# Kernel optimization log

Measured on AMD Instinct MI355X. Metric: run time of the kernel, lower is better.

## Reference

```python
import jax, jax.numpy as jnp
import numpy as np

NUM_GRAPHS = 128


def _gcn_layer(x, W, b, src, dst, out_norm, in_norm, n_nodes):
    # DGL GraphConv, norm='both': x * outdeg^{-1/2}, sum-aggregate src->dst, * indeg^{-1/2}, then @W + b
    x = x * out_norm[:, None]
    agg = jax.ops.segment_sum(x[src], dst, num_segments=n_nodes)  # [N, d]
    agg = agg * in_norm[:, None]
    return agg @ W + b


def setup_inputs() -> dict:
    key = jax.random.key(0)
    ks = jax.random.split(key, 10)
    N, E, D, H, P, C = 100000, 1600000, 128, 128, 64, 10
    h = jax.random.normal(ks[0], (N, D), dtype=jnp.float32)
    perm_features = jax.random.normal(ks[1], (NUM_GRAPHS, P), dtype=jnp.float32)
    W1 = jax.random.normal(ks[2], (D, H), dtype=jnp.float32) * (1.0 / np.sqrt(D))
    b1 = jnp.zeros((H,), dtype=jnp.float32)
    W2 = jax.random.normal(ks[3], (H, H), dtype=jnp.float32) * (1.0 / np.sqrt(H))
    b2 = jnp.zeros((H,), dtype=jnp.float32)
    Wc = jax.random.normal(ks[4], (H + P, C), dtype=jnp.float32) * (1.0 / np.sqrt(H + P))
    bc = jnp.zeros((C,), dtype=jnp.float32)
    src = jax.random.randint(ks[5], (E,), 0, N, dtype=jnp.int64)
    dst = jax.random.randint(ks[6], (E,), 0, N, dtype=jnp.int64)
    graph_ids = jnp.sort(jax.random.randint(ks[7], (N,), 0, NUM_GRAPHS, dtype=jnp.int64))
    return {"h": h, "perm_features": perm_features, "W1": W1, "b1": b1,
            "W2": W2, "b2": b2, "Wc": Wc, "bc": bc,
            "src": src, "dst": dst, "graph_ids": graph_ids}


def reference(h, perm_features, W1, b1, W2, b2, Wc, bc, src, dst, graph_ids):
    N = h.shape[0]
    ones_e = jnp.ones(src.shape[0], dtype=h.dtype)
    out_deg = jnp.maximum(jax.ops.segment_sum(ones_e, src, num_segments=N), 1.0)
    in_deg = jnp.maximum(jax.ops.segment_sum(ones_e, dst, num_segments=N), 1.0)
    out_norm = jax.lax.rsqrt(out_deg)
    in_norm = jax.lax.rsqrt(in_deg)

    x = _gcn_layer(h, W1, b1, src, dst, out_norm, in_norm, N)
    x = jax.nn.relu(x)
    x = _gcn_layer(x, W2, b2, src, dst, out_norm, in_norm, N)

    # dgl.mean_nodes: per-graph mean of node features
    sums = jax.ops.segment_sum(x, graph_ids, num_segments=NUM_GRAPHS)  # [G, H]
    counts = jnp.maximum(
        jax.ops.segment_sum(jnp.ones(N, dtype=x.dtype), graph_ids, num_segments=NUM_GRAPHS), 1.0)
    hg = sums / counts[:, None]

    combined = jnp.concatenate([hg, perm_features], axis=1)  # [G, H+P]
    return combined @ Wc + bc
```

## Files before the change

kernel.cpp:

```cpp
#include <hip/hip_runtime.h>


#define NUM_G 128
#define PB_EDGES 4096
#define W_BIN 128

typedef unsigned int uint32;
typedef short bf16x8 __attribute__((ext_vector_type(8)));
typedef float f32x4 __attribute__((ext_vector_type(4)));

__device__ __forceinline__ float bflo(uint32 u) { return __uint_as_float(u << 16); }
__device__ __forceinline__ float bfhi(uint32 u) { return __uint_as_float(u & 0xffff0000u); }
__device__ __forceinline__ uint32 f2bf_bits(float f) {
    uint32 b = __float_as_uint(f);
    return (b + 0x7fffu + ((b >> 16) & 1u)) >> 16;
}
__device__ __forceinline__ uint32 pack2(float a, float b) {
    return f2bf_bits(a) | (f2bf_bits(b) << 16);
}

__global__ __launch_bounds__(256) void p1_hist(const int* __restrict__ src,
                                               const int* __restrict__ dst, int E,
                                               int NBIN, int B, int* __restrict__ bh) {
    __shared__ int hist[1024];
    int b = blockIdx.x;
    int pipe = (b >= B) ? 1 : 0;
    int bb = pipe ? b - B : b;
    const int* key = pipe ? src : dst;
    for (int i = threadIdx.x; i < NBIN; i += 256) hist[i] = 0;
    __syncthreads();
    int base = bb * PB_EDGES;
    for (int c = threadIdx.x; c < PB_EDGES / 4; c += 256) {
        int e = base + c * 4;
        if (e + 3 < E) {
            int4 k4 = *(const int4*)(key + e);
            atomicAdd(&hist[k4.x >> 7], 1);
            atomicAdd(&hist[k4.y >> 7], 1);
            atomicAdd(&hist[k4.z >> 7], 1);
            atomicAdd(&hist[k4.w >> 7], 1);
        } else {
            for (int i = e; i < E && i < e + 4; i++) atomicAdd(&hist[key[i] >> 7], 1);
        }
    }
    __syncthreads();
    int* outp = bh + (size_t)pipe * NBIN * B;
    for (int k = threadIdx.x; k < NBIN; k += 256)
        outp[(size_t)k * B + bb] = hist[k];
}

__global__ __launch_bounds__(256) void p2a_tot(const int* __restrict__ bh, int NBIN, int B,
                                               int* __restrict__ tot) {
    __shared__ int sc[256];
    int k = blockIdx.x % NBIN, pipe = blockIdx.x / NBIN;
    const int* row = bh + (size_t)pipe * NBIN * B + (size_t)k * B;
    int acc = 0;
    for (int b = threadIdx.x; b < B; b += 256) acc += row[b];
    sc[threadIdx.x] = acc;
    __syncthreads();
    for (int o = 128; o > 0; o >>= 1) {
        if (threadIdx.x < o) sc[threadIdx.x] += sc[threadIdx.x + o];
        __syncthreads();
    }
    if (threadIdx.x == 0) tot[pipe * NBIN + k] = sc[0];
}

__global__ __launch_bounds__(512) void p2c_cursor(const int* __restrict__ bh,
                                                  const int* __restrict__ tot,
                                                  int NBIN, int B, int E,
                                                  int* __restrict__ bstart,
                                                  int* __restrict__ curs) {
    __shared__ int sc[512];
    int k = blockIdx.x % NBIN, pipe = blockIdx.x / NBIN;
    int i = threadIdx.x;
    int pacc = 0;
    for (int kk = i; kk < k; kk += 512) pacc += tot[pipe * NBIN + kk];
    sc[i] = pacc;
    __syncthreads();
    for (int o = 256; o > 0; o >>= 1) {
        if (i < o) sc[i] += sc[i + o];
        __syncthreads();
    }
    int base = sc[0];
    __syncthreads();
    if (i == 0) {
        bstart[pipe * (NBIN + 1) + k] = base;
        if (k == 0) bstart[pipe * (NBIN + 1) + NBIN] = E;
    }
    const int* row = bh + (size_t)pipe * NBIN * B + (size_t)k * B;
    int v = (i < B) ? row[i] : 0;
    sc[i] = v;
    __syncthreads();
    for (int o = 1; o < 512; o <<= 1) {
        int t = (i >= o) ? sc[i - o] : 0;
        __syncthreads();
        sc[i] += t;
        __syncthreads();
    }
    if (i < B)
        curs[(size_t)pipe * B * NBIN + (size_t)i * NBIN + k] = base + sc[i] - v;
}

__global__ __launch_bounds__(256) void p3_scatter(const int* __restrict__ src,
                                                  const int* __restrict__ dst, int E,
                                                  int NBIN, int B, const int* __restrict__ curs,
                                                  int* __restrict__ ebuf, int* __restrict__ sbuf) {
    __shared__ int cur[1024];
    int b = blockIdx.x;
    int pipe = (b >= B) ? 1 : 0;
    int bb = pipe ? b - B : b;
    const int* crow = curs + (size_t)pipe * B * NBIN + (size_t)bb * NBIN;
    for (int i = threadIdx.x; i < NBIN; i += 256) cur[i] = crow[i];
    __syncthreads();
    int base = bb * PB_EDGES;
    if (!pipe) {
        for (int c = threadIdx.x; c < PB_EDGES / 4; c += 256) {
            int e = base + c * 4;
            if (e + 3 < E) {
                int4 s4 = *(const int4*)(src + e);
                int4 d4 = *(const int4*)(dst + e);
                int p;
                p = atomicAdd(&cur[d4.x >> 7], 1); ebuf[p] = s4.x | ((d4.x & 127) << 17);
                p = atomicAdd(&cur[d4.y >> 7], 1); ebuf[p] = s4.y | ((d4.y & 127) << 17);
                p = atomicAdd(&cur[d4.z >> 7], 1); ebuf[p] = s4.z | ((d4.z & 127) << 17);
                p = atomicAdd(&cur[d4.w >> 7], 1); ebuf[p] = s4.w | ((d4.w & 127) << 17);
            } else {
                for (int i = e; i < E && i < e + 4; i++) {
                    int s = src[i], d = dst[i];
                    int p = atomicAdd(&cur[d >> 7], 1);
                    ebuf[p] = s | ((d & 127) << 17);
                }
            }
        }
    } else {
        for (int c = threadIdx.x; c < PB_EDGES / 4; c += 256) {
            int e = base + c * 4;
            if (e + 3 < E) {
                int4 s4 = *(const int4*)(src + e);
                int p;
                p = atomicAdd(&cur[s4.x >> 7], 1); sbuf[p] = s4.x;
                p = atomicAdd(&cur[s4.y >> 7], 1); sbuf[p] = s4.y;
                p = atomicAdd(&cur[s4.z >> 7], 1); sbuf[p] = s4.z;
                p = atomicAdd(&cur[s4.w >> 7], 1); sbuf[p] = s4.w;
            } else {
                for (int i = e; i < E && i < e + 4; i++) {
                    int s = src[i];
                    int p = atomicAdd(&cur[s >> 7], 1);
                    sbuf[p] = s;
                }
            }
        }
    }
}

__global__ __launch_bounds__(256) void p4_comb(const int* __restrict__ ebuf,
                                               const int* __restrict__ sbuf,
                                               const int* __restrict__ bstart,
                                               int NBIN, int N, int E,
                                               int* __restrict__ indeg, int* __restrict__ coff,
                                               int* __restrict__ adj, int* __restrict__ outdeg) {
    __shared__ int hist[128];
    __shared__ int sc[128];
    __shared__ int cur[128];
    __shared__ int lsrc[4096];
    int kb = blockIdx.x;
    int tid = threadIdx.x;
    if (kb >= NBIN) {
        int k = kb - NBIN;
        const int* bstartS = bstart + (NBIN + 1);
        int s0 = bstartS[k], s1 = bstartS[k + 1];
        if (tid < 128) hist[tid] = 0;
        __syncthreads();
        for (int i = s0 + tid; i < s1; i += 256) atomicAdd(&hist[sbuf[i] & 127], 1);
        __syncthreads();
        if (tid < 128) {
            int node = k * W_BIN + tid;
            if (node < N) outdeg[node] = hist[tid];
        }
        return;
    }
    int k = kb;
    int s0 = bstart[k], s1 = bstart[k + 1];
    int M = s1 - s0;
    if (tid < 128) hist[tid] = 0;
    __syncthreads();
    for (int i = tid; i < M; i += 256) {
        int e = ebuf[s0 + i];
        atomicAdd(&hist[(e >> 17) & 127], 1);
    }
    __syncthreads();
    if (tid < 128) sc[tid] = hist[tid];
    __syncthreads();
    for (int o = 1; o < 128; o <<= 1) {
        int v = 0;
        if (tid < 128 && tid >= o) v = sc[tid - o];
        __syncthreads();
        if (tid < 128) sc[tid] += v;
        __syncthreads();
    }
    if (tid < 128) {
        int node = k * W_BIN + tid;
        if (node < N) {
            indeg[node] = hist[tid];
            coff[node] = s0 + sc[tid] - hist[tid];
        }
        cur[tid] = sc[tid] - hist[tid];
    }
    if (k == NBIN - 1 && tid == 0) coff[N] = E;
    __syncthreads();
    if (M <= 4096) {
        for (int i = tid; i < M; i += 256) {
            int e = ebuf[s0 + i];
            int p = atomicAdd(&cur[(e >> 17) & 127], 1);
            lsrc[p] = e & 0x1FFFF;
        }
        __syncthreads();
        for (int i = tid; i < M; i += 256) adj[s0 + i] = lsrc[i];
    } else {
        for (int i = tid; i < M; i += 256) {
            int e = ebuf[s0 + i];
            int p = atomicAdd(&cur[(e >> 17) & 127], 1);
            adj[s0 + p] = e & 0x1FFFF;
        }
    }
}

__global__ void misc_kernel(const int* __restrict__ gids,
                            const int* __restrict__ outdeg, const int* __restrict__ indeg,
                            const float* __restrict__ W1, const float* __restrict__ W2,
                            int N, int* __restrict__ goffs,
                            float* __restrict__ nrm_out, float* __restrict__ nrm_in,
                            unsigned short* __restrict__ Wt1, unsigned short* __restrict__ Wt2) {
    int i = blockIdx.x * blockDim.x + threadIdx.x;
    if (i <= N) {
        int prev = (i == 0) ? -1 : gids[i - 1];
        int cur = (i == N) ? NUM_G : gids[i];
        for (int g = prev + 1; g <= cur && g <= NUM_G; g++) goffs[g] = i;
    }
    if (i < N) {
        nrm_out[i] = rsqrtf(fmaxf((float)outdeg[i], 1.0f));
        nrm_in[i]  = rsqrtf(fmaxf((float)indeg[i], 1.0f));
    }
    if (i < 32768) {
        int sel = i >> 14;
        int idx = i & 16383;
        int k = idx >> 7, n = idx & 127;
        float v = (sel ? W2 : W1)[idx];
        (sel ? Wt2 : Wt1)[n * 128 + k] = (unsigned short)f2bf_bits(v);
    }
}

__global__ void scale_kernel(const float* __restrict__ h, const float* __restrict__ nrm_out,
                             uint32* __restrict__ xsb, int N) {
    int t = blockIdx.x * blockDim.x + threadIdx.x;
    int node = t >> 4, q = t & 15;
    if (node >= N) return;
    float ns = nrm_out[node];
    const float4* hv = (const float4*)(h + (size_t)node * 128 + q * 8);
    float4 a = hv[0], b = hv[1];
    a.x *= ns; a.y *= ns; a.z *= ns; a.w *= ns;
    b.x *= ns; b.y *= ns; b.z *= ns; b.w *= ns;
    uint4 o;
    o.x = pack2(a.x, a.y); o.y = pack2(a.z, a.w);
    o.z = pack2(b.x, b.y); o.w = pack2(b.z, b.w);
    ((uint4*)xsb)[(size_t)node * 16 + q] = o;
}

__device__ __forceinline__ void acc8(float* acc, uint4 u) {
    acc[0] += bflo(u.x); acc[1] += bfhi(u.x); acc[2] += bflo(u.y); acc[3] += bfhi(u.y);
    acc[4] += bflo(u.z); acc[5] += bfhi(u.z); acc[6] += bflo(u.w); acc[7] += bfhi(u.w);
}

__global__ void agg_kernel(const uint32* __restrict__ xsb, const int* __restrict__ adj,
                           const int* __restrict__ coff, uint32* __restrict__ aggb, int N) {
    int t = blockIdx.x * blockDim.x + threadIdx.x;
    int node = t >> 4;
    int q = t & 15;
    if (node >= N) return;
    int jb = coff[node], je = coff[node + 1];
    float acc[8];
#pragma unroll
    for (int i = 0; i < 8; i++) acc[i] = 0.f;
    const uint4* rows = (const uint4*)xsb;
    int j = jb;
    for (; j + 7 < je; j += 8) {
        int s0 = adj[j], s1 = adj[j + 1], s2 = adj[j + 2], s3 = adj[j + 3];
        int s4 = adj[j + 4], s5 = adj[j + 5], s6 = adj[j + 6], s7 = adj[j + 7];
        uint4 u0 = rows[(size_t)s0 * 16 + q];
        uint4 u1 = rows[(size_t)s1 * 16 + q];
        uint4 u2 = rows[(size_t)s2 * 16 + q];
        uint4 u3 = rows[(size_t)s3 * 16 + q];
        uint4 u4 = rows[(size_t)s4 * 16 + q];
        uint4 u5 = rows[(size_t)s5 * 16 + q];
        uint4 u6 = rows[(size_t)s6 * 16 + q];
        uint4 u7 = rows[(size_t)s7 * 16 + q];
        acc8(acc, u0); acc8(acc, u1); acc8(acc, u2); acc8(acc, u3);
        acc8(acc, u4); acc8(acc, u5); acc8(acc, u6); acc8(acc, u7);
    }
    for (; j + 3 < je; j += 4) {
        int s0 = adj[j], s1 = adj[j + 1], s2 = adj[j + 2], s3 = adj[j + 3];
        uint4 u0 = rows[(size_t)s0 * 16 + q];
        uint4 u1 = rows[(size_t)s1 * 16 + q];
        uint4 u2 = rows[(size_t)s2 * 16 + q];
        uint4 u3 = rows[(size_t)s3 * 16 + q];
        acc8(acc, u0); acc8(acc, u1); acc8(acc, u2); acc8(acc, u3);
    }
    for (; j < je; j++) {
        uint4 u = rows[(size_t)adj[j] * 16 + q];
        acc8(acc, u);
    }
    uint4 o;
    o.x = pack2(acc[0], acc[1]); o.y = pack2(acc[2], acc[3]);
    o.z = pack2(acc[4], acc[5]); o.w = pack2(acc[6], acc[7]);
    ((uint4*)aggb)[(size_t)node * 16 + q] = o;
}

__global__ __launch_bounds__(256) void gemm_mfma(const unsigned short* __restrict__ A,
                                                 const unsigned short* __restrict__ Wtg,
                                                 const float* __restrict__ bias,
                                                 const float* __restrict__ rowscale,
                                                 const float* __restrict__ postscale,
                                                 unsigned short* __restrict__ out,
                                                 int N, int do_relu) {
    __shared__ unsigned short Wl[128 * 136];
    for (int i = threadIdx.x; i < 2048; i += 256) {
        uint4 v = ((const uint4*)Wtg)[i];
        *(uint4*)&Wl[(i >> 4) * 136 + (i & 15) * 8] = v;
    }
    __syncthreads();

    int lane = threadIdx.x & 63;
    int wv = threadIdx.x >> 6;
    int col_l = lane & 15;
    int quad = lane >> 4;
    int r0w = blockIdx.x * 128 + wv * 32;
    if (r0w >= N) return;

    int arow0 = r0w + col_l;        if (arow0 >= N) arow0 = N - 1;
    int arow1 = r0w + 16 + col_l;   if (arow1 >= N) arow1 = N - 1;
    const unsigned short* Ar0 = A + (size_t)arow0 * 128;
    const unsigned short* Ar1 = A + (size_t)arow1 * 128;

    f32x4 acc[2][8];
#pragma unroll
    for (int rt = 0; rt < 2; rt++)
#pragma unroll
        for (int t = 0; t < 8; t++) {
            acc[rt][t][0] = 0.f; acc[rt][t][1] = 0.f;
            acc[rt][t][2] = 0.f; acc[rt][t][3] = 0.f;
        }

#pragma unroll
    for (int kk = 0; kk < 4; kk++) {
        bf16x8 a0 = *(const bf16x8*)(Ar0 + kk * 32 + quad * 8);
        bf16x8 a1 = *(const bf16x8*)(Ar1 + kk * 32 + quad * 8);
        const unsigned short* wb = &Wl[(size_t)col_l * 136 + kk * 32 + quad * 8];
#pragma unroll
        for (int t = 0; t < 8; t++) {
            bf16x8 b = *(const bf16x8*)(wb + (size_t)t * 16 * 136);
            acc[0][t] = __builtin_amdgcn_mfma_f32_16x16x32_bf16(a0, b, acc[0][t], 0, 0, 0);
            acc[1][t] = __builtin_amdgcn_mfma_f32_16x16x32_bf16(a1, b, acc[1][t], 0, 0, 0);
        }
    }

#pragma unroll
    for (int rt = 0; rt < 2; rt++) {
        int rbase = r0w + rt * 16;
        float s[4], p[4];
#pragma unroll
        for (int j = 0; j < 4; j++) {
            int rw = rbase + quad * 4 + j;
            bool ok = rw < N;
            s[j] = ok ? rowscale[ok ? rw : 0] : 0.f;
            p[j] = (postscale != nullptr && ok) ? postscale[rw] : 1.f;
        }
#pragma unroll
        for (int t = 0; t < 8; t++) {
            int c = t * 16 + col_l;
            float bia = bias[c];
#pragma unroll
            for (int j = 0; j < 4; j++) {
                int rw = rbase + quad * 4 + j;
                if (rw >= N) continue;
                float v = fmaf(s[j], acc[rt][t][j], bia);
                if (do_relu) v = fmaxf(v, 0.f);
                v *= p[j];
                out[(size_t)rw * 128 + c] = (unsigned short)f2bf_bits(v);
            }
        }
    }
}

__global__ __launch_bounds__(1024) void mean_final(const uint32* __restrict__ x2b,
                                                   const int* __restrict__ goffs,
                                                   const float* __restrict__ perm,
                                                   const float* __restrict__ Wc,
                                                   const float* __restrict__ bc,
                                                   float* __restrict__ out) {
    __shared__ float red[16][128];
    __shared__ float hrow[128];
    int g = blockIdx.x;
    int cp = threadIdx.x & 63;
    int j = threadIdx.x >> 6;
    int s = goffs[g], e = goffs[g + 1];
    float a0 = 0.f, a1 = 0.f;
    for (int r = s + j; r < e; r += 16) {
        uint32 u = x2b[(size_t)r * 64 + cp];
        a0 += bflo(u); a1 += bfhi(u);
    }
    red[j][cp * 2] = a0;
    red[j][cp * 2 + 1] = a1;
    __syncthreads();
    if (j == 0) {
        float t0 = 0.f, t1 = 0.f;
#pragma unroll
        for (int jj = 0; jj < 16; jj++) { t0 += red[jj][cp * 2]; t1 += red[jj][cp * 2 + 1]; }
        float cnt = fmaxf((float)(e - s), 1.0f);
        hrow[cp * 2] = t0 / cnt;
        hrow[cp * 2 + 1] = t1 / cnt;
    }
    __syncthreads();
    if (threadIdx.x < 10) {
        int c = threadIdx.x;
        float acc = bc[c];
#pragma unroll 8
        for (int k = 0; k < 128; k++) acc = fmaf(hrow[k], Wc[k * 10 + c], acc);
        const float* prow = perm + g * 64;
#pragma unroll 8
        for (int p = 0; p < 64; p++) acc = fmaf(prow[p], Wc[(128 + p) * 10 + c], acc);
        out[g * 10 + c] = acc;
    }
}

extern "C" void kernel_launch(void* const* d_in, const int* in_sizes, int n_in,
                              void* d_out, int out_size, void* d_ws, size_t ws_size,
                              hipStream_t stream) {
    const float* h    = (const float*)d_in[0];
    const float* perm = (const float*)d_in[1];
    const float* W1   = (const float*)d_in[2];
    const float* b1   = (const float*)d_in[3];
    const float* W2   = (const float*)d_in[4];
    const float* b2   = (const float*)d_in[5];
    const float* Wc   = (const float*)d_in[6];
    const float* bc   = (const float*)d_in[7];
    const int* src    = (const int*)d_in[8];
    const int* dst    = (const int*)d_in[9];
    const int* gids   = (const int*)d_in[10];
    float* out = (float*)d_out;

    const int N = in_sizes[0] / 128;
    const int E = in_sizes[8];
    const int G = NUM_G, H = 128;
    const int B = (E + PB_EDGES - 1) / PB_EDGES;
    const int NBIN = (N + W_BIN - 1) / W_BIN;

    char* w = (char*)d_ws;
    size_t off = 0;
    auto alloc = [&](size_t bytes) -> void* {
        void* p = w + off;
        off = (off + bytes + 255) & ~(size_t)255;
        return p;
    };
    uint32* xsb   = (uint32*)alloc((size_t)N * H * 2);
    uint32* aggb  = (uint32*)alloc((size_t)N * H * 2);
    uint32* x1b   = (uint32*)alloc((size_t)N * H * 2);
    unsigned short* Wt1 = (unsigned short*)alloc(16384 * 2);
    unsigned short* Wt2 = (unsigned short*)alloc(16384 * 2);
    int*    adj     = (int*)alloc((size_t)E * 4);
    int*    coff    = (int*)alloc((size_t)(N + 1) * 4);
    int*    indeg   = (int*)alloc((size_t)N * 4);
    int*    outdeg  = (int*)alloc((size_t)N * 4);
    float*  nrm_out = (float*)alloc((size_t)N * 4);
    float*  nrm_in  = (float*)alloc((size_t)N * 4);
    int*    goffs   = (int*)alloc((size_t)(G + 1) * 4);

    char* tmp = (char*)aggb;
    size_t toff = 0;
    auto talloc = [&](size_t bytes) -> void* {
        void* p = tmp + toff;
        toff = (toff + bytes + 255) & ~(size_t)255;
        return p;
    };
    int*  ebuf   = (int*)talloc((size_t)E * 4);
    int*  sbuf   = (int*)talloc((size_t)E * 4);
    int*  bh     = (int*)talloc((size_t)2 * B * NBIN * 4);
    int*  curs   = (int*)talloc((size_t)2 * B * NBIN * 4);
    int*  tot    = (int*)talloc((size_t)2 * NBIN * 4);
    int*  bstart = (int*)talloc((size_t)2 * (NBIN + 1) * 4);

    p1_hist<<<2 * B, 256, 0, stream>>>(src, dst, E, NBIN, B, bh);
    p2a_tot<<<2 * NBIN, 256, 0, stream>>>(bh, NBIN, B, tot);
    p2c_cursor<<<2 * NBIN, 512, 0, stream>>>(bh, tot, NBIN, B, E, bstart, curs);
    p3_scatter<<<2 * B, 256, 0, stream>>>(src, dst, E, NBIN, B, curs, ebuf, sbuf);
    p4_comb<<<2 * NBIN, 256, 0, stream>>>(ebuf, sbuf, bstart, NBIN, N, E,
                                          indeg, coff, adj, outdeg);

    misc_kernel<<<(N + 1 + 255) / 256, 256, 0, stream>>>(gids, outdeg, indeg, W1, W2, N,
                                                         goffs, nrm_out, nrm_in, Wt1, Wt2);

    scale_kernel<<<(N * 16 + 255) / 256, 256, 0, stream>>>(h, nrm_out, xsb, N);
    agg_kernel<<<(N * 16 + 255) / 256, 256, 0, stream>>>(xsb, adj, coff, aggb, N);
    gemm_mfma<<<(N + 127) / 128, 256, 0, stream>>>((const unsigned short*)aggb, Wt1, b1,
                                                   nrm_in, nrm_out,
                                                   (unsigned short*)x1b, N, 1);

    agg_kernel<<<(N * 16 + 255) / 256, 256, 0, stream>>>(x1b, adj, coff, aggb, N);
    gemm_mfma<<<(N + 127) / 128, 256, 0, stream>>>((const unsigned short*)aggb, Wt2, b2,
                                                   nrm_in, nullptr,
                                                   (unsigned short*)xsb, N, 0);

    mean_final<<<G, 1024, 0, stream>>>(xsb, goffs, perm, Wc, bc, out);
}
```

Before: 353.1 us.

## Sort nodes by in-degree within bins to balance aggregation wavefronts

p4_comb now counting-sorts the nodes of each 128-node bin by in-degree (capped at 63) and writes a permutation, which agg_kernel uses to map threads to nodes. Nodes with similar degrees then share a wavefront, which reduces divergence from unequal neighbor-loop lengths. The 8-way unrolled gather loop is removed, leaving the 4-way loop, which lowers the number of loads in flight per thread. The permutation adds an indirection and scatters the output writes within each bin.

Measured after the change: 383.4 us. 1.09x slower.

```diff
diff --git a/kernel.cpp b/kernel.cpp
--- a/kernel.cpp
+++ b/kernel.cpp
@@ -157,11 +157,14 @@
                                                const int* __restrict__ bstart,
                                                int NBIN, int N, int E,
                                                int* __restrict__ indeg, int* __restrict__ coff,
-                                               int* __restrict__ adj, int* __restrict__ outdeg) {
+                                               int* __restrict__ adj, int* __restrict__ outdeg,
+                                               int* __restrict__ perm) {
     __shared__ int hist[128];
     __shared__ int sc[128];
     __shared__ int cur[128];
     __shared__ int lsrc[4096];
+    __shared__ int dcnt[64];
+    __shared__ int order[128];
     int kb = blockIdx.x;
     int tid = threadIdx.x;
     if (kb >= NBIN) {
@@ -182,6 +185,7 @@
     int s0 = bstart[k], s1 = bstart[k + 1];
     int M = s1 - s0;
     if (tid < 128) hist[tid] = 0;
+    if (tid < 64) dcnt[tid] = 0;
     __syncthreads();
     for (int i = tid; i < M; i += 256) {
         int e = ebuf[s0 + i];
@@ -197,6 +201,8 @@
         if (tid < 128) sc[tid] += v;
         __syncthreads();
     }
+    int valid = N - k * W_BIN;
+    if (valid > 128) valid = 128;
     if (tid < 128) {
         int node = k * W_BIN + tid;
         if (node < N) {
@@ -206,7 +212,23 @@
         cur[tid] = sc[tid] - hist[tid];
     }
     if (k == NBIN - 1 && tid == 0) coff[N] = E;
-    __syncthreads();
+    if (tid < valid) {
+        int key = hist[tid]; if (key > 63) key = 63;
+        atomicAdd(&dcnt[key], 1);
+    }
+    __syncthreads();
+    if (tid == 0) {
+        int a = 0;
+        for (int i = 0; i < 64; i++) { int t = dcnt[i]; dcnt[i] = a; a += t; }
+    }
+    __syncthreads();
+    if (tid < valid) {
+        int key = hist[tid]; if (key > 63) key = 63;
+        int p = atomicAdd(&dcnt[key], 1);
+        order[p] = tid;
+    }
+    __syncthreads();
+    if (tid < valid) perm[k * W_BIN + tid] = k * W_BIN + order[tid];
     if (M <= 4096) {
         for (int i = tid; i < M; i += 256) {
             int e = ebuf[s0 + i];
@@ -271,31 +293,19 @@
 }
 
 __global__ void agg_kernel(const uint32* __restrict__ xsb, const int* __restrict__ adj,
-                           const int* __restrict__ coff, uint32* __restrict__ aggb, int N) {
+                           const int* __restrict__ coff, const int* __restrict__ perm,
+                           uint32* __restrict__ aggb, int N) {
     int t = blockIdx.x * blockDim.x + threadIdx.x;
-    int node = t >> 4;
+    int gi = t >> 4;
     int q = t & 15;
-    if (node >= N) return;
+    if (gi >= N) return;
+    int node = perm[gi];
     int jb = coff[node], je = coff[node + 1];
     float acc[8];
 #pragma unroll
     for (int i = 0; i < 8; i++) acc[i] = 0.f;
     const uint4* rows = (const uint4*)xsb;
     int j = jb;
-    for (; j + 7 < je; j += 8) {
-        int s0 = adj[j], s1 = adj[j + 1], s2 = adj[j + 2], s3 = adj[j + 3];
-        int s4 = adj[j + 4], s5 = adj[j + 5], s6 = adj[j + 6], s7 = adj[j + 7];
-        uint4 u0 = rows[(size_t)s0 * 16 + q];
-        uint4 u1 = rows[(size_t)s1 * 16 + q];
-        uint4 u2 = rows[(size_t)s2 * 16 + q];
-        uint4 u3 = rows[(size_t)s3 * 16 + q];
-        uint4 u4 = rows[(size_t)s4 * 16 + q];
-        uint4 u5 = rows[(size_t)s5 * 16 + q];
-        uint4 u6 = rows[(size_t)s6 * 16 + q];
-        uint4 u7 = rows[(size_t)s7 * 16 + q];
-        acc8(acc, u0); acc8(acc, u1); acc8(acc, u2); acc8(acc, u3);
-        acc8(acc, u4); acc8(acc, u5); acc8(acc, u6); acc8(acc, u7);
-    }
     for (; j + 3 < je; j += 4) {
         int s0 = adj[j], s1 = adj[j + 1], s2 = adj[j + 2], s3 = adj[j + 3];
         uint4 u0 = rows[(size_t)s0 * 16 + q];
@@ -469,6 +479,7 @@
     int*    coff    = (int*)alloc((size_t)(N + 1) * 4);
     int*    indeg   = (int*)alloc((size_t)N * 4);
     int*    outdeg  = (int*)alloc((size_t)N * 4);
+    int*    nperm   = (int*)alloc((size_t)N * 4);
     float*  nrm_out = (float*)alloc((size_t)N * 4);
     float*  nrm_in  = (float*)alloc((size_t)N * 4);
     int*    goffs   = (int*)alloc((size_t)(G + 1) * 4);
@@ -492,18 +503,18 @@
     p2c_cursor<<<2 * NBIN, 512, 0, stream>>>(bh, tot, NBIN, B, E, bstart, curs);
     p3_scatter<<<2 * B, 256, 0, stream>>>(src, dst, E, NBIN, B, curs, ebuf, sbuf);
     p4_comb<<<2 * NBIN, 256, 0, stream>>>(ebuf, sbuf, bstart, NBIN, N, E,
-                                          indeg, coff, adj, outdeg);
+                                          indeg, coff, adj, outdeg, nperm);
 
     misc_kernel<<<(N + 1 + 255) / 256, 256, 0, stream>>>(gids, outdeg, indeg, W1, W2, N,
                                                          goffs, nrm_out, nrm_in, Wt1, Wt2);
 
     scale_kernel<<<(N * 16 + 255) / 256, 256, 0, stream>>>(h, nrm_out, xsb, N);
-    agg_kernel<<<(N * 16 + 255) / 256, 256, 0, stream>>>(xsb, adj, coff, aggb, N);
+    agg_kernel<<<(N * 16 + 255) / 256, 256, 0, stream>>>(xsb, adj, coff, nperm, aggb, N);
     gemm_mfma<<<(N + 127) / 128, 256, 0, stream>>>((const unsigned short*)aggb, Wt1, b1,
                                                    nrm_in, nrm_out,
                                                    (unsigned short*)x1b, N, 1);
 
-    agg_kernel<<<(N * 16 + 255) / 256, 256, 0, stream>>>(x1b, adj, coff, aggb, N);
+    agg_kernel<<<(N * 16 + 255) / 256, 256, 0, stream>>>(x1b, adj, coff, nperm, aggb, N);
     gemm_mfma<<<(N + 127) / 128, 256, 0, stream>>>((const unsigned short*)aggb, Wt2, b2,
                                                    nrm_in, nullptr,
                                                    (unsigned short*)xsb, N, 0);
```

## Fold misc kernel into histogram and combine kernels; drop 8-way gather unroll

Applied to the files above, without the earlier changes.

Removes the separate misc kernel. Graph offsets and the bf16 weight transposes are computed by extra blocks appended to the histogram launch, and the degree-to-rsqrt norms are written directly inside the combine kernel, so the int degree arrays are never stored or reread. This saves one launch and some global traffic. The aggregation kernel also drops its 8-edge unrolled loop, which leaves 4-edge batches as the widest form. That lowers register pressure but may expose less memory-level parallelism in the gather.

Result: no change. 347.7 us (-1.5%).

```diff
diff --git a/kernel.cpp b/kernel.cpp
--- a/kernel.cpp
+++ b/kernel.cpp
@@ -21,9 +21,35 @@
 
 __global__ __launch_bounds__(256) void p1_hist(const int* __restrict__ src,
                                                const int* __restrict__ dst, int E,
-                                               int NBIN, int B, int* __restrict__ bh) {
+                                               int NBIN, int B, int GB, int N,
+                                               const int* __restrict__ gids,
+                                               const float* __restrict__ W1,
+                                               const float* __restrict__ W2,
+                                               int* __restrict__ bh,
+                                               int* __restrict__ goffs,
+                                               unsigned short* __restrict__ Wt1,
+                                               unsigned short* __restrict__ Wt2) {
+    int b = blockIdx.x;
+    if (b >= 2 * B) {
+        int eb = b - 2 * B;
+        if (eb < GB) {
+            int i = eb * 256 + threadIdx.x;
+            if (i <= N) {
+                int prev = (i == 0) ? -1 : gids[i - 1];
+                int cur = (i == N) ? NUM_G : gids[i];
+                for (int g = prev + 1; g <= cur && g <= NUM_G; g++) goffs[g] = i;
+            }
+        } else {
+            int i = (eb - GB) * 256 + threadIdx.x;
+            int sel = i >> 14;
+            int idx = i & 16383;
+            int k = idx >> 7, n = idx & 127;
+            float v = (sel ? W2 : W1)[idx];
+            (sel ? Wt2 : Wt1)[n * 128 + k] = (unsigned short)f2bf_bits(v);
+        }
+        return;
+    }
     __shared__ int hist[1024];
-    int b = blockIdx.x;
     int pipe = (b >= B) ? 1 : 0;
     int bb = pipe ? b - B : b;
     const int* key = pipe ? src : dst;
@@ -156,8 +182,10 @@
                                                const int* __restrict__ sbuf,
                                                const int* __restrict__ bstart,
                                                int NBIN, int N, int E,
-                                               int* __restrict__ indeg, int* __restrict__ coff,
-                                               int* __restrict__ adj, int* __restrict__ outdeg) {
+                                               int* __restrict__ coff,
+                                               int* __restrict__ adj,
+                                               float* __restrict__ nrm_in,
+                                               float* __restrict__ nrm_out) {
     __shared__ int hist[128];
     __shared__ int sc[128];
     __shared__ int cur[128];
@@ -174,7 +202,7 @@
         __syncthreads();
         if (tid < 128) {
             int node = k * W_BIN + tid;
-            if (node < N) outdeg[node] = hist[tid];
+            if (node < N) nrm_out[node] = rsqrtf(fmaxf((float)hist[tid], 1.0f));
         }
         return;
     }
@@ -200,8 +228,8 @@
     if (tid < 128) {
         int node = k * W_BIN + tid;
         if (node < N) {
-            indeg[node] = hist[tid];
             coff[node] = s0 + sc[tid] - hist[tid];
+            nrm_in[node] = rsqrtf(fmaxf((float)hist[tid], 1.0f));
         }
         cur[tid] = sc[tid] - hist[tid];
     }
@@ -221,31 +249,6 @@
             int p = atomicAdd(&cur[(e >> 17) & 127], 1);
             adj[s0 + p] = e & 0x1FFFF;
         }
-    }
-}
-
-__global__ void misc_kernel(const int* __restrict__ gids,
-                            const int* __restrict__ outdeg, const int* __restrict__ indeg,
-                            const float* __restrict__ W1, const float* __restrict__ W2,
-                            int N, int* __restrict__ goffs,
-                            float* __restrict__ nrm_out, float* __restrict__ nrm_in,
-                            unsigned short* __restrict__ Wt1, unsigned short* __restrict__ Wt2) {
-    int i = blockIdx.x * blockDim.x + threadIdx.x;
-    if (i <= N) {
-        int prev = (i == 0) ? -1 : gids[i - 1];
-        int cur = (i == N) ? NUM_G : gids[i];
-        for (int g = prev + 1; g <= cur && g <= NUM_G; g++) goffs[g] = i;
-    }
-    if (i < N) {
-        nrm_out[i] = rsqrtf(fmaxf((float)outdeg[i], 1.0f));
-        nrm_in[i]  = rsqrtf(fmaxf((float)indeg[i], 1.0f));
-    }
-    if (i < 32768) {
-        int sel = i >> 14;
-        int idx = i & 16383;
-        int k = idx >> 7, n = idx & 127;
-        float v = (sel ? W2 : W1)[idx];
-        (sel ? Wt2 : Wt1)[n * 128 + k] = (unsigned short)f2bf_bits(v);
     }
 }
 
@@ -282,20 +285,6 @@
     for (int i = 0; i < 8; i++) acc[i] = 0.f;
     const uint4* rows = (const uint4*)xsb;
     int j = jb;
-    for (; j + 7 < je; j += 8) {
-        int s0 = adj[j], s1 = adj[j + 1], s2 = adj[j + 2], s3 = adj[j + 3];
-        int s4 = adj[j + 4], s5 = adj[j + 5], s6 = adj[j + 6], s7 = adj[j + 7];
-        uint4 u0 = rows[(size_t)s0 * 16 + q];
-        uint4 u1 = rows[(size_t)s1 * 16 + q];
-        uint4 u2 = rows[(size_t)s2 * 16 + q];
-        uint4 u3 = rows[(size_t)s3 * 16 + q];
-        uint4 u4 = rows[(size_t)s4 * 16 + q];
-        uint4 u5 = rows[(size_t)s5 * 16 + q];
-        uint4 u6 = rows[(size_t)s6 * 16 + q];
-        uint4 u7 = rows[(size_t)s7 * 16 + q];
-        acc8(acc, u0); acc8(acc, u1); acc8(acc, u2); acc8(acc, u3);
-        acc8(acc, u4); acc8(acc, u5); acc8(acc, u6); acc8(acc, u7);
-    }
     for (; j + 3 < je; j += 4) {
         int s0 = adj[j], s1 = adj[j + 1], s2 = adj[j + 2], s3 = adj[j + 3];
         uint4 u0 = rows[(size_t)s0 * 16 + q];
@@ -452,6 +441,7 @@
     const int G = NUM_G, H = 128;
     const int B = (E + PB_EDGES - 1) / PB_EDGES;
     const int NBIN = (N + W_BIN - 1) / W_BIN;
+    const int GB = (N + 1 + 255) / 256;
 
     char* w = (char*)d_ws;
     size_t off = 0;
@@ -467,8 +457,6 @@
     unsigned short* Wt2 = (unsigned short*)alloc(16384 * 2);
     int*    adj     = (int*)alloc((size_t)E * 4);
     int*    coff    = (int*)alloc((size_t)(N + 1) * 4);
-    int*    indeg   = (int*)alloc((size_t)N * 4);
-    int*    outdeg  = (int*)alloc((size_t)N * 4);
     float*  nrm_out = (float*)alloc((size_t)N * 4);
     float*  nrm_in  = (float*)alloc((size_t)N * 4);
     int*    goffs   = (int*)alloc((size_t)(G + 1) * 4);
@@ -487,15 +475,13 @@
     int*  tot    = (int*)talloc((size_t)2 * NBIN * 4);
     int*  bstart = (int*)talloc((size_t)2 * (NBIN + 1) * 4);
 
-    p1_hist<<<2 * B, 256, 0, stream>>>(src, dst, E, NBIN, B, bh);
+    p1_hist<<<2 * B + GB + 128, 256, 0, stream>>>(src, dst, E, NBIN, B, GB, N,
+                                                  gids, W1, W2, bh, goffs, Wt1, Wt2);
     p2a_tot<<<2 * NBIN, 256, 0, stream>>>(bh, NBIN, B, tot);
     p2c_cursor<<<2 * NBIN, 512, 0, stream>>>(bh, tot, NBIN, B, E, bstart, curs);
     p3_scatter<<<2 * B, 256, 0, stream>>>(src, dst, E, NBIN, B, curs, ebuf, sbuf);
     p4_comb<<<2 * NBIN, 256, 0, stream>>>(ebuf, sbuf, bstart, NBIN, N, E,
-                                          indeg, coff, adj, outdeg);
-
-    misc_kernel<<<(N + 1 + 255) / 256, 256, 0, stream>>>(gids, outdeg, indeg, W1, W2, N,
-                                                         goffs, nrm_out, nrm_in, Wt1, Wt2);
+                                          coff, adj, nrm_in, nrm_out);
 
     scale_kernel<<<(N * 16 + 255) / 256, 256, 0, stream>>>(h, nrm_out, xsb, N);
     agg_kernel<<<(N * 16 + 255) / 256, 256, 0, stream>>>(xsb, adj, coff, aggb, N);
```
